# Optimization experiments

Measured on AMD Instinct MI355X. Metric: run time of the kernel, lower is better.

## Reference

```python
import jax, jax.numpy as jnp
import numpy as np

N, E, R, D, L, B, K = 50000, 800000, 64, 64, 4, 2, 32


def setup_inputs() -> dict:
    ks = jax.random.split(jax.random.key(0), 10)
    return {
        "edge_index": jax.random.randint(ks[0], (2, E), 0, N),
        "edge_type": jax.random.randint(ks[1], (E,), 0, R),
        "h_index": jax.random.randint(ks[2], (B,), 0, N),
        "r_index": jax.random.randint(ks[3], (B,), 0, R),
        "t_index": jax.random.randint(ks[4], (B, K), 0, N),
        "rel_repr": jax.random.normal(ks[5], (B, R, D)) * 0.1,
        "boundary_extra": jax.random.normal(ks[6], (B, N, D)) * 0.02,
        "layers_W": jax.random.normal(ks[7], (L, 2 * D, D)) / np.sqrt(2 * D),
        "layers_b": jnp.zeros((L, D)),
        "ln_g": jnp.ones((L, D)),
        "ln_b": jnp.zeros((L, D)),
        "w1": jax.random.normal(ks[8], (2 * D, D)) / np.sqrt(2 * D),
        "b1": jnp.zeros((D,)),
        "w2": jax.random.normal(ks[9], (D,)) / np.sqrt(D),
        "b2": jnp.zeros((1,)),
    }


def _layer_norm(x, g, b, eps=1e-5):
    mu = x.mean(-1, keepdims=True)
    var = ((x - mu) ** 2).mean(-1, keepdims=True)
    return (x - mu) * jax.lax.rsqrt(var + eps) * g + b


def reference(edge_index, edge_type, h_index, r_index, t_index, rel_repr,
              boundary_extra, layers_W, layers_b, ln_g, ln_b, w1, b1, w2, b2):
    src, dst = edge_index[0], edge_index[1]
    query = rel_repr[jnp.arange(B), r_index]  # [B, D] per-query relation embedding
    # enhanced boundary: entity/relation-enhanced base + query injected at head node
    boundary = boundary_extra.at[jnp.arange(B), h_index].add(query)  # [B, N, D]
    seg = jax.vmap(lambda m: jax.ops.segment_sum(m, dst, num_segments=N))
    x = boundary
    for l in range(L):
        msg = x[:, src, :] * rel_repr[:, edge_type, :]   # DistMult messages [B, E, D]
        agg = seg(msg) + boundary                        # sum aggregation + boundary self-message
        out = jnp.einsum('bnd,df->bnf', jnp.concatenate([x, agg], -1), layers_W[l]) + layers_b[l]
        out = jax.nn.relu(_layer_norm(out, ln_g[l], ln_b[l]))
        x = out + x                                      # short_cut residual
    node_feat = jnp.concatenate(
        [x, jnp.broadcast_to(query[:, None, :], (B, N, D))], axis=-1)  # [B, N, 2D]
    feat = node_feat[jnp.arange(B)[:, None], t_index]    # gather tails [B, K, 2D]
    h = jax.nn.relu(feat @ w1 + b1)
    score = h @ w2 + b2                                  # [B, K]
    return score
```

## Files before the change

### kernel.cpp

```cpp
#include <hip/hip_runtime.h>
#include <hip/hip_bf16.h>

#define NN 50000
#define EE 800000
#define RR 64
#define DD 64
#define LL 4
#define BB 2
#define KK 32

#define NBUK 98
#define BROWS 512
#define CHUNK 2048
#define NBLK 391
#define PLACE_CAP 10240
#define CAP3 8192

#define PB_REL   0
#define PB_WT    8192
#define PB_LB    40960
#define PB_G     41216
#define PB_BETA  41472
#define PB_W1    41728
#define PB_B1    49920
#define PB_W2    49984
#define PB_B2    50048
#define PB_TOT   50049

typedef short v8s __attribute__((ext_vector_type(8)));
typedef float v4f __attribute__((ext_vector_type(4)));
typedef _Float16 v2h __attribute__((ext_vector_type(2)));
typedef _Float16 v4h __attribute__((ext_vector_type(4)));
typedef unsigned short v4u __attribute__((ext_vector_type(4)));

static __device__ __forceinline__ float ldany(const void* p, int i, int flag) {
    if (flag) return __bfloat162float(((const __hip_bfloat16*)p)[i]);
    return ((const float*)p)[i];
}
static __device__ __forceinline__ unsigned short tobf(float x) {
    return (unsigned short)(__builtin_bit_cast(unsigned int, x) >> 16);
}
static __device__ __forceinline__ unsigned short rnebf(float x) {
    unsigned int u = __builtin_bit_cast(unsigned int, x);
    return (unsigned short)((u + 0x7FFFu + ((u >> 16) & 1u)) >> 16);
}
static __device__ __forceinline__ float frombf(unsigned short h) {
    return __builtin_bit_cast(float, ((unsigned int)h) << 16);
}
static __device__ __forceinline__ int getflag(const unsigned int* lng) {
    return (*lng == 0x3F803F80u) ? 1 : 0;
}

__global__ void k_prep(const void* __restrict__ rel, const void* __restrict__ lb,
                       const void* __restrict__ g, const void* __restrict__ beta,
                       const void* __restrict__ w1, const void* __restrict__ b1,
                       const void* __restrict__ w2, const void* __restrict__ b2,
                       const void* __restrict__ W, const unsigned int* __restrict__ lng,
                       float* __restrict__ pb, unsigned short* __restrict__ wshi,
                       unsigned short* __restrict__ wslo, _Float16* __restrict__ relH,
                       int* __restrict__ bucketCount, int* __restrict__ flag2,
                       int* __restrict__ flag3, int* __restrict__ cnts) {
    int gid = blockIdx.x * 256 + threadIdx.x;
    int flag = getflag(lng);
    if (gid < NBUK) bucketCount[gid] = 0;
    if (gid < NN) { flag2[gid] = 0; flag3[gid] = 0; }
    if (gid < 8) cnts[gid] = 0;
    if (gid < 32768) {
        int l = gid >> 13, r = gid & 8191, f = r >> 7, d = r & 127;
        float w = ldany(W, l * 8192 + d * 64 + f, flag);
        unsigned short h = tobf(w);
        wshi[gid] = h;
        wslo[gid] = tobf(w - frombf(h));
        if (gid < 8192) {
            int ty = gid >> 7, rr = gid & 127, dd = rr >> 1, b = rr & 1;
            relH[gid] = (_Float16)ldany(rel, b * 4096 + ty * 64 + dd, flag);
        }
    }
    if (gid >= PB_TOT) return;
    if (gid < PB_WT) { pb[gid] = ldany(rel, gid, flag); return; }
    if (gid < PB_LB) return;
    if (gid < PB_G)    { pb[gid] = ldany(lb,   gid - PB_LB,   flag); return; }
    if (gid < PB_BETA) { pb[gid] = ldany(g,    gid - PB_G,    flag); return; }
    if (gid < PB_W1)   { pb[gid] = ldany(beta, gid - PB_BETA, flag); return; }
    if (gid < PB_B1)   { pb[gid] = ldany(w1,   gid - PB_W1,   flag); return; }
    if (gid < PB_W2)   { pb[gid] = ldany(b1,   gid - PB_B1,   flag); return; }
    if (gid < PB_B2)   { pb[gid] = ldany(w2,   gid - PB_W2,   flag); return; }
    pb[gid] = ldany(b2, 0, flag);
}

__global__ void __launch_bounds__(256) k_bhist(const int* __restrict__ ei,
                                               int* __restrict__ bucketCount) {
    __shared__ int h[NBUK];
    int t = threadIdx.x;
    if (t < NBUK) h[t] = 0;
    __syncthreads();
    int base = blockIdx.x * CHUNK;
    #pragma unroll
    for (int i = 0; i < 8; ++i) {
        int e = base + i * 256 + t;
        if (e < EE) atomicAdd(&h[ei[EE + e] >> 9], 1);
    }
    __syncthreads();
    if (t < NBUK && h[t]) atomicAdd(&bucketCount[t], h[t]);
}

__global__ void k_bscan(const int* __restrict__ bucketCount,
                        int* __restrict__ bucketBase, int* __restrict__ bucketCursor) {
    __shared__ int s[128];
    int t = threadIdx.x;
    int v = (t < NBUK) ? bucketCount[t] : 0;
    s[t] = v;
    __syncthreads();
    for (int off = 1; off < 128; off <<= 1) {
        int a = (t >= off) ? s[t - off] : 0;
        __syncthreads();
        if (t >= off) s[t] += a;
        __syncthreads();
    }
    if (t < NBUK) {
        int b = s[t] - v;
        bucketBase[t] = b;
        bucketCursor[t] = b;
    }
    if (t == NBUK - 1) bucketBase[NBUK] = s[t];
}

__global__ void __launch_bounds__(256) k_bfill(const int* __restrict__ ei,
                                               const int* __restrict__ et,
                                               int* __restrict__ bucketCursor,
                                               unsigned int* __restrict__ btmp) {
    __shared__ int h[NBUK], rb[NBUK];
    int t = threadIdx.x;
    if (t < NBUK) h[t] = 0;
    __syncthreads();
    int base = blockIdx.x * CHUNK;
    unsigned int rec[8]; int bk[8];
    #pragma unroll
    for (int i = 0; i < 8; ++i) {
        int e = base + i * 256 + t;
        bk[i] = -1;
        if (e < EE) {
            int dst = ei[EE + e];
            rec[i] = (unsigned int)ei[e] | ((unsigned int)et[e] << 16)
                   | ((unsigned int)(dst & 511) << 22);
            bk[i] = dst >> 9;
            atomicAdd(&h[bk[i]], 1);
        }
    }
    __syncthreads();
    if (t < NBUK) rb[t] = h[t] ? atomicAdd(&bucketCursor[t], h[t]) : 0;
    __syncthreads();
    if (t < NBUK) h[t] = 0;
    __syncthreads();
    #pragma unroll
    for (int i = 0; i < 8; ++i) {
        if (bk[i] >= 0) {
            int pos = rb[bk[i]] + atomicAdd(&h[bk[i]], 1);
            btmp[pos] = rec[i];
        }
    }
}

__global__ void __launch_bounds__(256) k_place(const int* __restrict__ bucketBase,
                                               const unsigned int* __restrict__ btmp,
                                               unsigned int* __restrict__ elist,
                                               int* __restrict__ rowptr) {
    __shared__ int rp[BROWS + 1];
    __shared__ int cur[BROWS];
    __shared__ unsigned int outb[PLACE_CAP];
    int b = blockIdx.x, t = threadIdx.x;
    int base = bucketBase[b];
    int cnt  = bucketBase[b + 1] - base;

    for (int r = t; r < BROWS; r += 256) cur[r] = 0;
    __syncthreads();
    for (int i = t; i < cnt; i += 256) {
        unsigned int rec = btmp[base + i];
        atomicAdd(&cur[rec >> 22], 1);
    }
    __syncthreads();
    if (t < 64) {
        int lane = t;
        int loc[8]; int s = 0;
        #pragma unroll
        for (int j = 0; j < 8; ++j) { loc[j] = s; s += cur[lane * 8 + j]; }
        int inc = s;
        for (int off = 1; off < 64; off <<= 1) {
            int v = __shfl_up(inc, off, 64);
            if (lane >= off) inc += v;
        }
        int excl = inc - s;
        #pragma unroll
        for (int j = 0; j < 8; ++j) rp[lane * 8 + j] = excl + loc[j];
        if (lane == 63) rp[BROWS] = inc;
    }
    __syncthreads();
    for (int r = t; r < BROWS; r += 256) cur[r] = rp[r];
    __syncthreads();
    for (int i = t; i < cnt; i += 256) {
        unsigned int rec = btmp[base + i];
        int ld = rec >> 22;
        int pos = atomicAdd(&cur[ld], 1);
        outb[pos] = rec & 0x3FFFFFu;
    }
    __syncthreads();
    for (int i = t; i < cnt; i += 256) elist[base + i] = outb[i];
    for (int r = t; r < BROWS; r += 256) {
        int n = b * BROWS + r;
        if (n <= NN) rowptr[n] = base + rp[r];
    }
}

__global__ void k_setT(const int* __restrict__ t_index, int* __restrict__ flag3,
                       int* __restrict__ listT, int* __restrict__ cntT,
                       int* __restrict__ list3, int* __restrict__ cnt3) {
    int i = threadIdx.x;
    int t = t_index[i];
    if (atomicExch(&flag3[t], 1) == 0) {
        listT[atomicAdd(cntT, 1)] = t;
        list3[atomicAdd(cnt3, 1)] = t;
    }
}

__global__ void __launch_bounds__(256) k_set3(const int* __restrict__ rowptr,
                                              const unsigned int* __restrict__ elist,
                                              const int* __restrict__ listT,
                                              const int* __restrict__ cntT,
                                              int* __restrict__ flag3,
                                              int* __restrict__ list3,
                                              int* __restrict__ cnt3) {
    int wave = threadIdx.x >> 6, lane = threadIdx.x & 63;
    int idx = blockIdx.x * 4 + wave;
    if (idx >= *cntT) return;
    int n = listT[idx];
    int s0 = rowptr[n], s1 = rowptr[n + 1];
    for (int i = s0 + lane; i < s1; i += 64) {
        int src = (int)(elist[i] & 0xFFFFu);
        if (atomicExch(&flag3[src], 1) == 0) {
            int p = atomicAdd(cnt3, 1);
            if (p < CAP3) list3[p] = src;
        }
    }
}

__global__ void __launch_bounds__(256) k_set2(const int* __restrict__ rowptr,
                                              const unsigned int* __restrict__ elist,
                                              const int* __restrict__ list3,
                                              const int* __restrict__ cnt3,
                                              int* __restrict__ flag2,
                                              int* __restrict__ list2,
                                              int* __restrict__ cnt2) {
    int wave = threadIdx.x >> 6, lane = threadIdx.x & 63;
    int nw = gridDim.x * 4;
    int c3 = *cnt3;
    for (int idx = blockIdx.x * 4 + wave; idx < c3; idx += nw) {
        int n = list3[idx];
        if (lane == 0) {
            if (atomicExch(&flag2[n], 1) == 0) list2[atomicAdd(cnt2, 1)] = n;
        }
        int s0 = rowptr[n], s1 = rowptr[n + 1];
        for (int i = s0 + lane; i < s1; i += 64) {
            int src = (int)(elist[i] & 0xFFFFu);
            if (atomicExch(&flag2[src], 1) == 0) {
                list2[atomicAdd(cnt2, 1)] = src;
            }
        }
    }
}

__global__ void k_init(const void* __restrict__ be, const float* __restrict__ relf,
                       const int* __restrict__ h_index, const int* __restrict__ r_index,
                       const unsigned int* __restrict__ lng, _Float16* __restrict__ xH) {
    int idx = blockIdx.x * 256 + threadIdx.x;
    int flag = getflag(lng);
    int bn = idx >> 6;
    int d  = idx & 63;
    int b  = (bn >= NN) ? 1 : 0;
    int n  = bn - b * NN;
    float v = ldany(be, idx, flag);
    if (n == h_index[b]) v += relf[(b * RR + r_index[b]) * DD + d];
    xH[n * 128 + d * 2 + b] = (_Float16)v;
}

__global__ void __launch_bounds__(256) k_gather(const int* __restrict__ rowptr,
                                                const unsigned int* __restrict__ elist,
                                                const _Float16* __restrict__ xHin,
                                                const _Float16* __restrict__ relH,
                                                const void* __restrict__ be,
                                                const float* __restrict__ relf,
                                                const int* __restrict__ h_index,
                                                const int* __restrict__ r_index,
                                                const unsigned int* __restrict__ lng,
                                                const int* __restrict__ list,
                                                const int* __restrict__ cntp,
                                                unsigned short* __restrict__ aggH) {
    int wave = threadIdx.x >> 6, lane = threadIdx.x & 63;
    int idx = blockIdx.x * 4 + wave;
    int cnt = cntp ? *cntp : NN;
    if (idx >= cnt) return;
    int n = list ? list[idx] : idx;
    n = __builtin_amdgcn_readfirstlane(n);
    int start = __builtin_amdgcn_readfirstlane(rowptr[n]);
    int end   = __builtin_amdgcn_readfirstlane(rowptr[n + 1]);
    int flag  = getflag(lng);

    float a0 = ldany(be, n * DD + lane, flag);
    float a1 = ldany(be, (NN + n) * DD + lane, flag);
    if (n == h_index[0]) a0 += relf[(0 * RR + r_index[0]) * DD + lane];
    if (n == h_index[1]) a1 += relf[(1 * RR + r_index[1]) * DD + lane];

    for (int i = start; i < end; i += 8) {
        v2h xv[8], rv[8]; float mk[8];
        #pragma unroll
        for (int j = 0; j < 8; ++j) {
            int e = i + j;
            int ok = (e < end);
            unsigned int u = elist[ok ? e : start];
            int s = u & 0xFFFFu, ty = u >> 16;
            xv[j] = *(const v2h*)(xHin + s * 128 + lane * 2);
            rv[j] = *(const v2h*)(relH + ty * 128 + lane * 2);
            mk[j] = ok ? 1.f : 0.f;
        }
        #pragma unroll
        for (int j = 0; j < 8; ++j) {
            a0 += (float)xv[j].x * (float)rv[j].x * mk[j];
            a1 += (float)xv[j].y * (float)rv[j].y * mk[j];
        }
    }
    aggH[n * 64 + lane] = rnebf(a0);
    aggH[(NN + n) * 64 + lane] = rnebf(a1);
}

__global__ void __launch_bounds__(256) k_combine(const _Float16* __restrict__ xHin,
                                                 const unsigned short* __restrict__ aggH,
                                                 const unsigned short* __restrict__ whi,
                                                 const unsigned short* __restrict__ wlo,
                                                 const float* __restrict__ lb,
                                                 const float* __restrict__ g,
                                                 const float* __restrict__ beta,
                                                 const int* __restrict__ list,
                                                 const int* __restrict__ cntp,
                                                 _Float16* __restrict__ xHout) {
    __shared__ __attribute__((aligned(16))) unsigned short Xhi[64 * 136];
    __shared__ __attribute__((aligned(16))) unsigned short Xlo[64 * 72];
    __shared__ int nodes[32];
    float* outT = (float*)Xhi;

    int t = threadIdx.x;
    int cnt = cntp ? *cntp : NN;
    int ebase = blockIdx.x * 32;
    if (ebase >= cnt) return;

    if (t < 32) {
        int e = ebase + t;
        int ce = e < cnt ? e : cnt - 1;
        nodes[t] = list ? list[ce] : ce;
    }
    __syncthreads();

    #pragma unroll
    for (int it = 0; it < 4; ++it) {
        int idx = it * 256 + t;
        int nl = idx >> 5, j = idx & 31;
        int n = nodes[nl];
        v4h v = *(const v4h*)(xHin + (size_t)n * 128 + 4 * j);
        int r0 = nl, r1 = 32 + nl;
        int k0 = 2 * j, k1 = 2 * j + 1;
        float f; unsigned short h;
        f = (float)v.x; h = tobf(f); Xhi[r0 * 136 + k0] = h; Xlo[r0 * 72 + k0] = tobf(f - frombf(h));
        f = (float)v.y; h = tobf(f); Xhi[r1 * 136 + k0] = h; Xlo[r1 * 72 + k0] = tobf(f - frombf(h));
        f = (float)v.z; h = tobf(f); Xhi[r0 * 136 + k1] = h; Xlo[r0 * 72 + k1] = tobf(f - frombf(h));
        f = (float)v.w; h = tobf(f); Xhi[r1 * 136 + k1] = h; Xlo[r1 * 72 + k1] = tobf(f - frombf(h));
    }
    #pragma unroll
    for (int it = 0; it < 4; ++it) {
        int idx = it * 256 + t;
        int half = idx >> 9, rem = idx & 511;
        int nl = rem >> 4, j = rem & 15;
        int n = nodes[nl];
        v4u v = *(const v4u*)(aggH + (size_t)(half * NN + n) * 64 + 4 * j);
        int row = half * 32 + nl;
        int kb = 64 + 4 * j;
        Xhi[row * 136 + kb + 0] = v.x;
        Xhi[row * 136 + kb + 1] = v.y;
        Xhi[row * 136 + kb + 2] = v.z;
        Xhi[row * 136 + kb + 3] = v.w;
    }
    __syncthreads();

    int wave = t >> 6, lane = t & 63;
    int low = lane & 15, q = lane >> 4;

    v4f acc[4];
    #pragma unroll
    for (int ft = 0; ft < 4; ++ft) acc[ft] = 0.f;

    int arow = wave * 16 + low;
    #pragma unroll
    for (int kt = 0; kt < 2; ++kt) {
        int k0 = kt * 32 + q * 8;
        v8s ah = *(const v8s*)(Xhi + arow * 136 + k0);
        v8s al = *(const v8s*)(Xlo + arow * 72 + k0);
        #pragma unroll
        for (int ft = 0; ft < 4; ++ft) {
            v8s bh = *(const v8s*)(whi + (ft * 16 + low) * 128 + k0);
            v8s bl = *(const v8s*)(wlo + (ft * 16 + low) * 128 + k0);
            acc[ft] = __builtin_amdgcn_mfma_f32_16x16x32_bf16(ah, bh, acc[ft], 0, 0, 0);
            acc[ft] = __builtin_amdgcn_mfma_f32_16x16x32_bf16(al, bh, acc[ft], 0, 0, 0);
            acc[ft] = __builtin_amdgcn_mfma_f32_16x16x32_bf16(ah, bl, acc[ft], 0, 0, 0);
        }
    }
    #pragma unroll
    for (int kt = 2; kt < 4; ++kt) {
        int k0 = kt * 32 + q * 8;
        v8s ah = *(const v8s*)(Xhi + arow * 136 + k0);
        #pragma unroll
        for (int ft = 0; ft < 4; ++ft) {
            v8s bh = *(const v8s*)(whi + (ft * 16 + low) * 128 + k0);
            v8s bl = *(const v8s*)(wlo + (ft * 16 + low) * 128 + k0);
            acc[ft] = __builtin_amdgcn_mfma_f32_16x16x32_bf16(ah, bh, acc[ft], 0, 0, 0);
            acc[ft] = __builtin_amdgcn_mfma_f32_16x16x32_bf16(ah, bl, acc[ft], 0, 0, 0);
        }
    }

    float o[4][4];
    #pragma unroll
    for (int ft = 0; ft < 4; ++ft) {
        float lbv = lb[ft * 16 + low];
        #pragma unroll
        for (int r = 0; r < 4; ++r) o[ft][r] = acc[ft][r] + lbv;
    }
    float s1[4], s2[4];
    #pragma unroll
    for (int r = 0; r < 4; ++r) {
        s1[r] = o[0][r] + o[1][r] + o[2][r] + o[3][r];
        s2[r] = o[0][r]*o[0][r] + o[1][r]*o[1][r] + o[2][r]*o[2][r] + o[3][r]*o[3][r];
    }
    #pragma unroll
    for (int m = 1; m < 16; m <<= 1) {
        #pragma unroll
        for (int r = 0; r < 4; ++r) {
            s1[r] += __shfl_xor(s1[r], m, 64);
            s2[r] += __shfl_xor(s2[r], m, 64);
        }
    }
    float res[4][4];
    #pragma unroll
    for (int r = 0; r < 4; ++r) {
        int row = wave * 16 + q * 4 + r;
        float mu  = s1[r] * (1.f / 64.f);
        float var = s2[r] * (1.f / 64.f) - mu * mu;
        float rs  = rsqrtf(fmaxf(var, 0.f) + 1e-5f);
        #pragma unroll
        for (int ft = 0; ft < 4; ++ft) {
            int f = ft * 16 + low;
            float xold = frombf(Xhi[row * 136 + f]) + frombf(Xlo[row * 72 + f]);
            res[ft][r] = fmaxf((o[ft][r] - mu) * rs * g[f] + beta[f], 0.f) + xold;
        }
    }
    __syncthreads();

    #pragma unroll
    for (int r = 0; r < 4; ++r) {
        int row = wave * 16 + q * 4 + r;
        #pragma unroll
        for (int ft = 0; ft < 4; ++ft) outT[row * 65 + ft * 16 + low] = res[ft][r];
    }
    __syncthreads();

    #pragma unroll
    for (int it = 0; it < 4; ++it) {
        int idx = it * 256 + t;
        int nl = idx >> 5, j = idx & 31;
        if (ebase + nl < cnt) {
            int n = nodes[nl];
            v4h hv;
            hv.x = (_Float16)outT[nl * 65 + 2 * j];
            hv.y = (_Float16)outT[(32 + nl) * 65 + 2 * j];
            hv.z = (_Float16)outT[nl * 65 + 2 * j + 1];
            hv.w = (_Float16)outT[(32 + nl) * 65 + 2 * j + 1];
            *(v4h*)(xHout + (size_t)n * 128 + 4 * j) = hv;
        }
    }
}

__global__ void k_final(const _Float16* __restrict__ xH,
                        const float* __restrict__ relf,
                        const int* __restrict__ r_index,
                        const int* __restrict__ t_index,
                        const float* __restrict__ w1,
                        const float* __restrict__ b1,
                        const float* __restrict__ w2,
                        const float* __restrict__ b2,
                        const unsigned int* __restrict__ lng,
                        void* __restrict__ out) {
    int b = blockIdx.x >> 5;
    int k = blockIdx.x & 31;
    int f = threadIdx.x;
    int t = t_index[b * KK + k];
    const _Float16* xr = xH + (size_t)t * 128 + b;
    const float* q  = relf + (b * RR + r_index[b]) * DD;
    float acc = b1[f];
    #pragma unroll 8
    for (int d = 0; d < 64; ++d) acc += (float)xr[2 * d] * w1[d * 64 + f];
    #pragma unroll 8
    for (int d = 0; d < 64; ++d) acc += q[d] * w1[(64 + d) * 64 + f];
    float h = fmaxf(acc, 0.f);
    float p = h * w2[f];
    for (int m = 32; m > 0; m >>= 1) p += __shfl_xor(p, m, 64);
    if (f == 0) {
        float s = p + b2[0];
        if (getflag(lng)) ((__hip_bfloat16*)out)[b * KK + k] = __float2bfloat16(s);
        else              ((float*)out)[b * KK + k] = s;
    }
}

extern "C" void kernel_launch(void* const* d_in, const int* in_sizes, int n_in,
                              void* d_out, int out_size, void* d_ws, size_t ws_size,
                              hipStream_t stream) {
    const int* edge_index = (const int*)d_in[0];
    const int* edge_type  = (const int*)d_in[1];
    const int* h_index    = (const int*)d_in[2];
    const int* r_index    = (const int*)d_in[3];
    const int* t_index    = (const int*)d_in[4];
    const void* rel   = d_in[5];
    const void* be    = d_in[6];
    const void* lw    = d_in[7];
    const void* lbias = d_in[8];
    const void* lng   = d_in[9];
    const void* lnb   = d_in[10];
    const void* w1    = d_in[11];
    const void* b1    = d_in[12];
    const void* w2    = d_in[13];
    const void* b2    = d_in[14];

    _Float16* xHa = (_Float16*)d_ws;
    _Float16* xHb = xHa + (size_t)NN * 128;
    unsigned short* aggH = (unsigned short*)(xHb + (size_t)NN * 128);
    float*    pb  = (float*)(aggH + (size_t)BB * NN * 64);
    int*      ip  = (int*)(pb + PB_TOT);
    int*   rowptr       = ip;
    int*   bucketCount  = rowptr + NN + 1;
    int*   bucketBase   = bucketCount + NBUK;
    int*   bucketCursor = bucketBase + NBUK + 1;
    unsigned int* elist = (unsigned int*)(bucketCursor + NBUK);
    unsigned short* wshi = (unsigned short*)(elist + EE);
    unsigned short* wslo = wshi + 32768;
    _Float16* relH = (_Float16*)(wslo + 32768);
    int* flag2 = (int*)(relH + 8192);
    int* flag3 = flag2 + NN;
    int* listT = flag3 + NN;
    int* list3 = listT + 64;
    int* list2 = list3 + CAP3;
    int* cnts  = list2 + NN;
    unsigned int* btmp = (unsigned int*)xHb;
    const unsigned int* lngp = (const unsigned int*)lng;

    k_prep<<<196, 256, 0, stream>>>(rel, lbias, lng, lnb, w1, b1, w2, b2, lw,
                                    lngp, pb, wshi, wslo, relH, bucketCount,
                                    flag2, flag3, cnts);
    k_bhist<<<NBLK, 256, 0, stream>>>(edge_index, bucketCount);
    k_bscan<<<1, 128, 0, stream>>>(bucketCount, bucketBase, bucketCursor);
    k_bfill<<<NBLK, 256, 0, stream>>>(edge_index, edge_type, bucketCursor, btmp);
    k_place<<<NBUK, 256, 0, stream>>>(bucketBase, btmp, elist, rowptr);
    k_setT<<<1, 64, 0, stream>>>(t_index, flag3, listT, cnts + 0, list3, cnts + 1);
    k_set3<<<16, 256, 0, stream>>>(rowptr, elist, listT, cnts + 0, flag3, list3, cnts + 1);
    k_set2<<<256, 256, 0, stream>>>(rowptr, elist, list3, cnts + 1, flag2, list2, cnts + 2);
    k_init<<<25000, 256, 0, stream>>>(be, pb + PB_REL, h_index, r_index, lngp, xHa);

    const float* relf = pb + PB_REL;
    k_gather<<<12500, 256, 0, stream>>>(rowptr, elist, xHa, relH, be, relf,
                                        h_index, r_index, lngp, nullptr, nullptr, aggH);
    k_combine<<<1563, 256, 0, stream>>>(xHa, aggH, wshi + 0, wslo + 0,
                                        pb + PB_LB + 0, pb + PB_G + 0, pb + PB_BETA + 0,
                                        nullptr, nullptr, xHb);
    k_gather<<<12500, 256, 0, stream>>>(rowptr, elist, xHb, relH, be, relf,
                                        h_index, r_index, lngp, list2, cnts + 2, aggH);
    k_combine<<<1563, 256, 0, stream>>>(xHb, aggH, wshi + 8192, wslo + 8192,
                                        pb + PB_LB + 64, pb + PB_G + 64, pb + PB_BETA + 64,
                                        list2, cnts + 2, xHa);
    k_gather<<<2048, 256, 0, stream>>>(rowptr, elist, xHa, relH, be, relf,
                                       h_index, r_index, lngp, list3, cnts + 1, aggH);
    k_combine<<<256, 256, 0, stream>>>(xHa, aggH, wshi + 16384, wslo + 16384,
                                       pb + PB_LB + 128, pb + PB_G + 128, pb + PB_BETA + 128,
                                       list3, cnts + 1, xHb);
    k_gather<<<16, 256, 0, stream>>>(rowptr, elist, xHb, relH, be, relf,
                                     h_index, r_index, lngp, listT, cnts + 0, aggH);
    k_combine<<<2, 256, 0, stream>>>(xHb, aggH, wshi + 24576, wslo + 24576,
                                     pb + PB_LB + 192, pb + PB_G + 192, pb + PB_BETA + 192,
                                     listT, cnts + 0, xHa);
    k_final<<<64, 64, 0, stream>>>(xHa, pb + PB_REL, r_index, t_index,
                                   pb + PB_W1, pb + PB_B1, pb + PB_W2, pb + PB_B2,
                                   lngp, d_out);
}
```

Before: 340.9 us.

## Replace bucketed CSR build with degree-count scan and atomic scatter; fuse init into prep

Replaces the two-level bucket sort (histogram, bucket scan, bucket fill, per-bucket placement) with a per-node degree count, a three-pass prefix scan, and a direct atomic-cursor scatter into the edge list. The degree count and the vectorized boundary/x initialization are folded into the prep kernel as extra blocks. The two target-set kernels are merged into one, and flags are cleared with a memset. This cuts kernel launches and passes over the edges, but global atomics on per-node cursors give a nondeterministic edge order within each row and may contend more.

```diff
diff --git a/kernel.cpp b/kernel.cpp
--- a/kernel.cpp
+++ b/kernel.cpp
@@ -9,12 +9,13 @@
 #define BB 2
 #define KK 32
 
-#define NBUK 98
-#define BROWS 512
 #define CHUNK 2048
 #define NBLK 391
-#define PLACE_CAP 10240
 #define CAP3 8192
+
+#define PREP_BLKS 196
+#define INIT_BLKS 3125
+#define DEG_BLKS  391
 
 #define PB_REL   0
 #define PB_WT    8192
@@ -31,6 +32,7 @@
 typedef float v4f __attribute__((ext_vector_type(4)));
 typedef _Float16 v2h __attribute__((ext_vector_type(2)));
 typedef _Float16 v4h __attribute__((ext_vector_type(4)));
+typedef _Float16 v8h __attribute__((ext_vector_type(8)));
 typedef unsigned short v4u __attribute__((ext_vector_type(4)));
 
 static __device__ __forceinline__ float ldany(const void* p, int i, int flag) {
@@ -51,20 +53,65 @@
     return (*lng == 0x3F803F80u) ? 1 : 0;
 }
 
-__global__ void k_prep(const void* __restrict__ rel, const void* __restrict__ lb,
+__global__ void __launch_bounds__(256) k_prep(const void* __restrict__ rel, const void* __restrict__ lb,
                        const void* __restrict__ g, const void* __restrict__ beta,
                        const void* __restrict__ w1, const void* __restrict__ b1,
                        const void* __restrict__ w2, const void* __restrict__ b2,
                        const void* __restrict__ W, const unsigned int* __restrict__ lng,
+                       const void* __restrict__ be,
+                       const int* __restrict__ h_index, const int* __restrict__ r_index,
+                       const int* __restrict__ ei,
                        float* __restrict__ pb, unsigned short* __restrict__ wshi,
                        unsigned short* __restrict__ wslo, _Float16* __restrict__ relH,
-                       int* __restrict__ bucketCount, int* __restrict__ flag2,
-                       int* __restrict__ flag3, int* __restrict__ cnts) {
-    int gid = blockIdx.x * 256 + threadIdx.x;
+                       _Float16* __restrict__ xH, int* __restrict__ deg) {
+    int blk = blockIdx.x, t = threadIdx.x;
     int flag = getflag(lng);
-    if (gid < NBUK) bucketCount[gid] = 0;
-    if (gid < NN) { flag2[gid] = 0; flag3[gid] = 0; }
-    if (gid < 8) cnts[gid] = 0;
+
+    if (blk >= PREP_BLKS + INIT_BLKS) {
+        int base = (blk - PREP_BLKS - INIT_BLKS) * CHUNK;
+        #pragma unroll
+        for (int i = 0; i < 8; ++i) {
+            int e = base + i * 256 + t;
+            if (e < EE) atomicAdd(&deg[ei[EE + e]], 1);
+        }
+        return;
+    }
+    if (blk >= PREP_BLKS) {
+        int gid = (blk - PREP_BLKS) * 256 + t;
+        int n = gid >> 4, j = gid & 15, d0 = j * 4;
+        float x0[4], x1[4];
+        if (flag) {
+            v4u a = *(const v4u*)((const unsigned short*)be + (size_t)n * 64 + d0);
+            v4u bq = *(const v4u*)((const unsigned short*)be + (size_t)(NN + n) * 64 + d0);
+            #pragma unroll
+            for (int jj = 0; jj < 4; ++jj) { x0[jj] = frombf(a[jj]); x1[jj] = frombf(bq[jj]); }
+        } else {
+            v4f a = *(const v4f*)((const float*)be + (size_t)n * 64 + d0);
+            v4f bq = *(const v4f*)((const float*)be + (size_t)(NN + n) * 64 + d0);
+            #pragma unroll
+            for (int jj = 0; jj < 4; ++jj) { x0[jj] = a[jj]; x1[jj] = bq[jj]; }
+        }
+        if (n == h_index[0]) {
+            int r = r_index[0];
+            #pragma unroll
+            for (int jj = 0; jj < 4; ++jj) x0[jj] += ldany(rel, r * DD + d0 + jj, flag);
+        }
+        if (n == h_index[1]) {
+            int r = r_index[1];
+            #pragma unroll
+            for (int jj = 0; jj < 4; ++jj) x1[jj] += ldany(rel, (RR + r) * DD + d0 + jj, flag);
+        }
+        v8h o;
+        #pragma unroll
+        for (int jj = 0; jj < 4; ++jj) {
+            o[2 * jj]     = (_Float16)x0[jj];
+            o[2 * jj + 1] = (_Float16)x1[jj];
+        }
+        *(v8h*)(xH + (size_t)n * 128 + d0 * 2) = o;
+        return;
+    }
+
+    int gid = blk * 256 + t;
     if (gid < 32768) {
         int l = gid >> 13, r = gid & 8191, f = r >> 7, d = r & 127;
         float w = ldany(W, l * 8192 + d * 64 + f, flag);
@@ -88,159 +135,108 @@
     pb[gid] = ldany(b2, 0, flag);
 }
 
-__global__ void __launch_bounds__(256) k_bhist(const int* __restrict__ ei,
-                                               int* __restrict__ bucketCount) {
-    __shared__ int h[NBUK];
-    int t = threadIdx.x;
-    if (t < NBUK) h[t] = 0;
-    __syncthreads();
-    int base = blockIdx.x * CHUNK;
-    #pragma unroll
-    for (int i = 0; i < 8; ++i) {
-        int e = base + i * 256 + t;
-        if (e < EE) atomicAdd(&h[ei[EE + e] >> 9], 1);
-    }
-    __syncthreads();
-    if (t < NBUK && h[t]) atomicAdd(&bucketCount[t], h[t]);
-}
-
-__global__ void k_bscan(const int* __restrict__ bucketCount,
-                        int* __restrict__ bucketBase, int* __restrict__ bucketCursor) {
-    __shared__ int s[128];
-    int t = threadIdx.x;
-    int v = (t < NBUK) ? bucketCount[t] : 0;
+__global__ void __launch_bounds__(256) k_scan1(const int* __restrict__ deg,
+                                               int* __restrict__ cursor,
+                                               int* __restrict__ bsum) {
+    __shared__ int s[256];
+    int b = blockIdx.x, t = threadIdx.x;
+    int n = b * 256 + t;
+    int v = (n < NN) ? deg[n] : 0;
     s[t] = v;
     __syncthreads();
-    for (int off = 1; off < 128; off <<= 1) {
+    for (int off = 1; off < 256; off <<= 1) {
         int a = (t >= off) ? s[t - off] : 0;
         __syncthreads();
         if (t >= off) s[t] += a;
         __syncthreads();
     }
-    if (t < NBUK) {
-        int b = s[t] - v;
-        bucketBase[t] = b;
-        bucketCursor[t] = b;
-    }
-    if (t == NBUK - 1) bucketBase[NBUK] = s[t];
-}
-
-__global__ void __launch_bounds__(256) k_bfill(const int* __restrict__ ei,
-                                               const int* __restrict__ et,
-                                               int* __restrict__ bucketCursor,
-                                               unsigned int* __restrict__ btmp) {
-    __shared__ int h[NBUK], rb[NBUK];
+    if (n < NN) cursor[n] = s[t] - v;
+    if (t == 255) bsum[b] = s[255];
+}
+
+__global__ void k_scan2(const int* __restrict__ bsum, int* __restrict__ boff,
+                        int* __restrict__ rowptr) {
+    __shared__ int s[256];
     int t = threadIdx.x;
-    if (t < NBUK) h[t] = 0;
-    __syncthreads();
+    int v = (t < PREP_BLKS) ? bsum[t] : 0;
+    s[t] = v;
+    __syncthreads();
+    for (int off = 1; off < 256; off <<= 1) {
+        int a = (t >= off) ? s[t - off] : 0;
+        __syncthreads();
+        if (t >= off) s[t] += a;
+        __syncthreads();
+    }
+    if (t < PREP_BLKS) boff[t] = s[t] - v;
+    if (t == 0) rowptr[NN] = EE;
+}
+
+__global__ void __launch_bounds__(256) k_scan3(int* __restrict__ cursor,
+                                               const int* __restrict__ boff,
+                                               int* __restrict__ rowptr) {
+    int b = blockIdx.x, t = threadIdx.x;
+    int n = b * 256 + t;
+    if (n < NN) {
+        int r = cursor[n] + boff[b];
+        rowptr[n] = r;
+        cursor[n] = r;
+    }
+}
+
+__global__ void __launch_bounds__(256) k_scatter(const int* __restrict__ ei,
+                                                 const int* __restrict__ et,
+                                                 int* __restrict__ cursor,
+                                                 unsigned int* __restrict__ elist) {
+    int t = threadIdx.x;
     int base = blockIdx.x * CHUNK;
-    unsigned int rec[8]; int bk[8];
     #pragma unroll
     for (int i = 0; i < 8; ++i) {
         int e = base + i * 256 + t;
-        bk[i] = -1;
         if (e < EE) {
             int dst = ei[EE + e];
-            rec[i] = (unsigned int)ei[e] | ((unsigned int)et[e] << 16)
-                   | ((unsigned int)(dst & 511) << 22);
-            bk[i] = dst >> 9;
-            atomicAdd(&h[bk[i]], 1);
-        }
-    }
-    __syncthreads();
-    if (t < NBUK) rb[t] = h[t] ? atomicAdd(&bucketCursor[t], h[t]) : 0;
-    __syncthreads();
-    if (t < NBUK) h[t] = 0;
-    __syncthreads();
-    #pragma unroll
-    for (int i = 0; i < 8; ++i) {
-        if (bk[i] >= 0) {
-            int pos = rb[bk[i]] + atomicAdd(&h[bk[i]], 1);
-            btmp[pos] = rec[i];
-        }
-    }
-}
-
-__global__ void __launch_bounds__(256) k_place(const int* __restrict__ bucketBase,
-                                               const unsigned int* __restrict__ btmp,
-                                               unsigned int* __restrict__ elist,
-                                               int* __restrict__ rowptr) {
-    __shared__ int rp[BROWS + 1];
-    __shared__ int cur[BROWS];
-    __shared__ unsigned int outb[PLACE_CAP];
-    int b = blockIdx.x, t = threadIdx.x;
-    int base = bucketBase[b];
-    int cnt  = bucketBase[b + 1] - base;
-
-    for (int r = t; r < BROWS; r += 256) cur[r] = 0;
-    __syncthreads();
-    for (int i = t; i < cnt; i += 256) {
-        unsigned int rec = btmp[base + i];
-        atomicAdd(&cur[rec >> 22], 1);
-    }
+            unsigned int rec = (unsigned int)ei[e] | ((unsigned int)et[e] << 16);
+            int pos = atomicAdd(&cursor[dst], 1);
+            elist[pos] = rec;
+        }
+    }
+}
+
+__global__ void k_sets(const int* __restrict__ t_index,
+                       const int* __restrict__ rowptr,
+                       const unsigned int* __restrict__ elist,
+                       int* __restrict__ flag3,
+                       int* __restrict__ listT, int* __restrict__ list3,
+                       int* __restrict__ cnts) {
+    __shared__ int sT, s3;
+    __shared__ int lT[64];
+    int t = threadIdx.x;
+    if (t == 0) { sT = 0; s3 = 0; }
     __syncthreads();
     if (t < 64) {
-        int lane = t;
-        int loc[8]; int s = 0;
-        #pragma unroll
-        for (int j = 0; j < 8; ++j) { loc[j] = s; s += cur[lane * 8 + j]; }
-        int inc = s;
-        for (int off = 1; off < 64; off <<= 1) {
-            int v = __shfl_up(inc, off, 64);
-            if (lane >= off) inc += v;
-        }
-        int excl = inc - s;
-        #pragma unroll
-        for (int j = 0; j < 8; ++j) rp[lane * 8 + j] = excl + loc[j];
-        if (lane == 63) rp[BROWS] = inc;
-    }
-    __syncthreads();
-    for (int r = t; r < BROWS; r += 256) cur[r] = rp[r];
-    __syncthreads();
-    for (int i = t; i < cnt; i += 256) {
-        unsigned int rec = btmp[base + i];
-        int ld = rec >> 22;
-        int pos = atomicAdd(&cur[ld], 1);
-        outb[pos] = rec & 0x3FFFFFu;
-    }
-    __syncthreads();
-    for (int i = t; i < cnt; i += 256) elist[base + i] = outb[i];
-    for (int r = t; r < BROWS; r += 256) {
-        int n = b * BROWS + r;
-        if (n <= NN) rowptr[n] = base + rp[r];
-    }
-}
-
-__global__ void k_setT(const int* __restrict__ t_index, int* __restrict__ flag3,
-                       int* __restrict__ listT, int* __restrict__ cntT,
-                       int* __restrict__ list3, int* __restrict__ cnt3) {
-    int i = threadIdx.x;
-    int t = t_index[i];
-    if (atomicExch(&flag3[t], 1) == 0) {
-        listT[atomicAdd(cntT, 1)] = t;
-        list3[atomicAdd(cnt3, 1)] = t;
-    }
-}
-
-__global__ void __launch_bounds__(256) k_set3(const int* __restrict__ rowptr,
-                                              const unsigned int* __restrict__ elist,
-                                              const int* __restrict__ listT,
-                                              const int* __restrict__ cntT,
-                                              int* __restrict__ flag3,
-                                              int* __restrict__ list3,
-                                              int* __restrict__ cnt3) {
-    int wave = threadIdx.x >> 6, lane = threadIdx.x & 63;
-    int idx = blockIdx.x * 4 + wave;
-    if (idx >= *cntT) return;
-    int n = listT[idx];
-    int s0 = rowptr[n], s1 = rowptr[n + 1];
-    for (int i = s0 + lane; i < s1; i += 64) {
-        int src = (int)(elist[i] & 0xFFFFu);
-        if (atomicExch(&flag3[src], 1) == 0) {
-            int p = atomicAdd(cnt3, 1);
-            if (p < CAP3) list3[p] = src;
-        }
-    }
+        int n = t_index[t];
+        if (atomicExch(&flag3[n], 1) == 0) {
+            int p = atomicAdd(&sT, 1);
+            lT[p] = n; listT[p] = n; list3[p] = n;
+        }
+    }
+    __syncthreads();
+    int nT = sT;
+    if (t == 0) s3 = nT;
+    __syncthreads();
+    int wave = t >> 6, lane = t & 63;
+    for (int idx = wave; idx < nT; idx += 4) {
+        int n = lT[idx];
+        int s0 = rowptr[n], s1 = rowptr[n + 1];
+        for (int i = s0 + lane; i < s1; i += 64) {
+            int src = (int)(elist[i] & 0xFFFFu);
+            if (atomicExch(&flag3[src], 1) == 0) {
+                int p = atomicAdd(&s3, 1);
+                if (p < CAP3) list3[p] = src;
+            }
+        }
+    }
+    __syncthreads();
+    if (t == 0) { cnts[0] = nT; cnts[1] = (s3 > CAP3) ? CAP3 : s3; }
 }
 
 __global__ void __launch_bounds__(256) k_set2(const int* __restrict__ rowptr,
@@ -266,20 +262,6 @@
             }
         }
     }
-}
-
-__global__ void k_init(const void* __restrict__ be, const float* __restrict__ relf,
-                       const int* __restrict__ h_index, const int* __restrict__ r_index,
-                       const unsigned int* __restrict__ lng, _Float16* __restrict__ xH) {
-    int idx = blockIdx.x * 256 + threadIdx.x;
-    int flag = getflag(lng);
-    int bn = idx >> 6;
-    int d  = idx & 63;
-    int b  = (bn >= NN) ? 1 : 0;
-    int n  = bn - b * NN;
-    float v = ldany(be, idx, flag);
-    if (n == h_index[b]) v += relf[(b * RR + r_index[b]) * DD + d];
-    xH[n * 128 + d * 2 + b] = (_Float16)v;
 }
 
 __global__ void __launch_bounds__(256) k_gather(const int* __restrict__ rowptr,
@@ -539,34 +521,33 @@
     unsigned short* aggH = (unsigned short*)(xHb + (size_t)NN * 128);
     float*    pb  = (float*)(aggH + (size_t)BB * NN * 64);
     int*      ip  = (int*)(pb + PB_TOT);
-    int*   rowptr       = ip;
-    int*   bucketCount  = rowptr + NN + 1;
-    int*   bucketBase   = bucketCount + NBUK;
-    int*   bucketCursor = bucketBase + NBUK + 1;
-    unsigned int* elist = (unsigned int*)(bucketCursor + NBUK);
+    int* deg    = ip;
+    int* flag2  = deg + NN;
+    int* flag3  = flag2 + NN;
+    int* cnts   = flag3 + NN;
+    int* rowptr = cnts + 16;
+    int* cursor = rowptr + NN + 1;
+    int* bsum   = cursor + NN;
+    int* boff   = bsum + 256;
+    int* listT  = boff + 256;
+    int* list3  = listT + 64;
+    int* list2  = list3 + CAP3;
+    unsigned int* elist = (unsigned int*)(list2 + NN);
     unsigned short* wshi = (unsigned short*)(elist + EE);
     unsigned short* wslo = wshi + 32768;
     _Float16* relH = (_Float16*)(wslo + 32768);
-    int* flag2 = (int*)(relH + 8192);
-    int* flag3 = flag2 + NN;
-    int* listT = flag3 + NN;
-    int* list3 = listT + 64;
-    int* list2 = list3 + CAP3;
-    int* cnts  = list2 + NN;
-    unsigned int* btmp = (unsigned int*)xHb;
     const unsigned int* lngp = (const unsigned int*)lng;
 
-    k_prep<<<196, 256, 0, stream>>>(rel, lbias, lng, lnb, w1, b1, w2, b2, lw,
-                                    lngp, pb, wshi, wslo, relH, bucketCount,
-                                    flag2, flag3, cnts);
-    k_bhist<<<NBLK, 256, 0, stream>>>(edge_index, bucketCount);
-    k_bscan<<<1, 128, 0, stream>>>(bucketCount, bucketBase, bucketCursor);
-    k_bfill<<<NBLK, 256, 0, stream>>>(edge_index, edge_type, bucketCursor, btmp);
-    k_place<<<NBUK, 256, 0, stream>>>(bucketBase, btmp, elist, rowptr);
-    k_setT<<<1, 64, 0, stream>>>(t_index, flag3, listT, cnts + 0, list3, cnts + 1);
-    k_set3<<<16, 256, 0, stream>>>(rowptr, elist, listT, cnts + 0, flag3, list3, cnts + 1);
+    hipMemsetAsync(deg, 0, (size_t)(3 * NN + 16) * sizeof(int), stream);
+    k_prep<<<PREP_BLKS + INIT_BLKS + DEG_BLKS, 256, 0, stream>>>(
+        rel, lbias, lng, lnb, w1, b1, w2, b2, lw, lngp, be, h_index, r_index,
+        edge_index, pb, wshi, wslo, relH, xHa, deg);
+    k_scan1<<<PREP_BLKS, 256, 0, stream>>>(deg, cursor, bsum);
+    k_scan2<<<1, 256, 0, stream>>>(bsum, boff, rowptr);
+    k_scan3<<<PREP_BLKS, 256, 0, stream>>>(cursor, boff, rowptr);
+    k_scatter<<<NBLK, 256, 0, stream>>>(edge_index, edge_type, cursor, elist);
+    k_sets<<<1, 256, 0, stream>>>(t_index, rowptr, elist, flag3, listT, list3, cnts);
     k_set2<<<256, 256, 0, stream>>>(rowptr, elist, list3, cnts + 1, flag2, list2, cnts + 2);
-    k_init<<<25000, 256, 0, stream>>>(be, pb + PB_REL, h_index, r_index, lngp, xHa);
 
     const float* relf = pb + PB_REL;
     k_gather<<<12500, 256, 0, stream>>>(rowptr, elist, xHa, relH, be, relf,
```

Result: slower. 394.0 us (+15.6%).

## Merge prep, init and histogram kernels; fuse set kernels; use memset for zeroing

Applied to the files above, without the earlier changes.

Folds the boundary initialization (k_init) and the edge destination histogram (k_bhist) into k_prep as extra block ranges, and vectorizes the init so each thread writes 8 fp16 values instead of one. The k_setT and k_set3 kernels are merged into a single one-block kernel that uses shared-memory counters. Flag and counter zeroing moves to one hipMemsetAsync over a reordered workspace layout. The aim is to cut kernel launch count and per-launch gaps and to widen the init memory traffic. The trade-off is that set3 now runs on one block with four waves instead of sixteen blocks.

```diff
diff --git a/kernel.cpp b/kernel.cpp
--- a/kernel.cpp
+++ b/kernel.cpp
@@ -15,6 +15,10 @@
 #define NBLK 391
 #define PLACE_CAP 10240
 #define CAP3 8192
+
+#define PREP_BLKS 196
+#define INIT_BLKS 3125
+#define HIST_BLKS 391
 
 #define PB_REL   0
 #define PB_WT    8192
@@ -31,6 +35,7 @@
 typedef float v4f __attribute__((ext_vector_type(4)));
 typedef _Float16 v2h __attribute__((ext_vector_type(2)));
 typedef _Float16 v4h __attribute__((ext_vector_type(4)));
+typedef _Float16 v8h __attribute__((ext_vector_type(8)));
 typedef unsigned short v4u __attribute__((ext_vector_type(4)));
 
 static __device__ __forceinline__ float ldany(const void* p, int i, int flag) {
@@ -51,26 +56,76 @@
     return (*lng == 0x3F803F80u) ? 1 : 0;
 }
 
-__global__ void k_prep(const void* __restrict__ rel, const void* __restrict__ lb,
+__global__ void __launch_bounds__(256) k_prep(const void* __restrict__ rel, const void* __restrict__ lb,
                        const void* __restrict__ g, const void* __restrict__ beta,
                        const void* __restrict__ w1, const void* __restrict__ b1,
                        const void* __restrict__ w2, const void* __restrict__ b2,
                        const void* __restrict__ W, const unsigned int* __restrict__ lng,
+                       const void* __restrict__ be,
+                       const int* __restrict__ h_index, const int* __restrict__ r_index,
+                       const int* __restrict__ ei,
                        float* __restrict__ pb, unsigned short* __restrict__ wshi,
                        unsigned short* __restrict__ wslo, _Float16* __restrict__ relH,
-                       int* __restrict__ bucketCount, int* __restrict__ flag2,
-                       int* __restrict__ flag3, int* __restrict__ cnts) {
-    int gid = blockIdx.x * 256 + threadIdx.x;
+                       _Float16* __restrict__ xH, int* __restrict__ bucketCount) {
+    __shared__ int h[NBUK];
+    int blk = blockIdx.x, t = threadIdx.x;
     int flag = getflag(lng);
-    if (gid < NBUK) bucketCount[gid] = 0;
-    if (gid < NN) { flag2[gid] = 0; flag3[gid] = 0; }
-    if (gid < 8) cnts[gid] = 0;
+
+    if (blk >= PREP_BLKS + INIT_BLKS) {
+        if (t < NBUK) h[t] = 0;
+        __syncthreads();
+        int base = (blk - PREP_BLKS - INIT_BLKS) * CHUNK;
+        #pragma unroll
+        for (int i = 0; i < 8; ++i) {
+            int e = base + i * 256 + t;
+            if (e < EE) atomicAdd(&h[ei[EE + e] >> 9], 1);
+        }
+        __syncthreads();
+        if (t < NBUK && h[t]) atomicAdd(&bucketCount[t], h[t]);
+        return;
+    }
+    if (blk >= PREP_BLKS) {
+        int gid = (blk - PREP_BLKS) * 256 + t;
+        int n = gid >> 4, j = gid & 15, d0 = j * 4;
+        float x0[4], x1[4];
+        if (flag) {
+            v4u a = *(const v4u*)((const unsigned short*)be + (size_t)n * 64 + d0);
+            v4u bq = *(const v4u*)((const unsigned short*)be + (size_t)(NN + n) * 64 + d0);
+            #pragma unroll
+            for (int jj = 0; jj < 4; ++jj) { x0[jj] = frombf(a[jj]); x1[jj] = frombf(bq[jj]); }
+        } else {
+            v4f a = *(const v4f*)((const float*)be + (size_t)n * 64 + d0);
+            v4f bq = *(const v4f*)((const float*)be + (size_t)(NN + n) * 64 + d0);
+            #pragma unroll
+            for (int jj = 0; jj < 4; ++jj) { x0[jj] = a[jj]; x1[jj] = bq[jj]; }
+        }
+        if (n == h_index[0]) {
+            int r = r_index[0];
+            #pragma unroll
+            for (int jj = 0; jj < 4; ++jj) x0[jj] += ldany(rel, r * DD + d0 + jj, flag);
+        }
+        if (n == h_index[1]) {
+            int r = r_index[1];
+            #pragma unroll
+            for (int jj = 0; jj < 4; ++jj) x1[jj] += ldany(rel, (RR + r) * DD + d0 + jj, flag);
+        }
+        v8h o;
+        #pragma unroll
+        for (int jj = 0; jj < 4; ++jj) {
+            o[2 * jj]     = (_Float16)x0[jj];
+            o[2 * jj + 1] = (_Float16)x1[jj];
+        }
+        *(v8h*)(xH + (size_t)n * 128 + d0 * 2) = o;
+        return;
+    }
+
+    int gid = blk * 256 + t;
     if (gid < 32768) {
         int l = gid >> 13, r = gid & 8191, f = r >> 7, d = r & 127;
         float w = ldany(W, l * 8192 + d * 64 + f, flag);
-        unsigned short h = tobf(w);
-        wshi[gid] = h;
-        wslo[gid] = tobf(w - frombf(h));
+        unsigned short h2 = tobf(w);
+        wshi[gid] = h2;
+        wslo[gid] = tobf(w - frombf(h2));
         if (gid < 8192) {
             int ty = gid >> 7, rr = gid & 127, dd = rr >> 1, b = rr & 1;
             relH[gid] = (_Float16)ldany(rel, b * 4096 + ty * 64 + dd, flag);
@@ -88,22 +143,6 @@
     pb[gid] = ldany(b2, 0, flag);
 }
 
-__global__ void __launch_bounds__(256) k_bhist(const int* __restrict__ ei,
-                                               int* __restrict__ bucketCount) {
-    __shared__ int h[NBUK];
-    int t = threadIdx.x;
-    if (t < NBUK) h[t] = 0;
-    __syncthreads();
-    int base = blockIdx.x * CHUNK;
-    #pragma unroll
-    for (int i = 0; i < 8; ++i) {
-        int e = base + i * 256 + t;
-        if (e < EE) atomicAdd(&h[ei[EE + e] >> 9], 1);
-    }
-    __syncthreads();
-    if (t < NBUK && h[t]) atomicAdd(&bucketCount[t], h[t]);
-}
-
 __global__ void k_bscan(const int* __restrict__ bucketCount,
                         int* __restrict__ bucketBase, int* __restrict__ bucketCursor) {
     __shared__ int s[128];
@@ -211,36 +250,42 @@
     }
 }
 
-__global__ void k_setT(const int* __restrict__ t_index, int* __restrict__ flag3,
-                       int* __restrict__ listT, int* __restrict__ cntT,
-                       int* __restrict__ list3, int* __restrict__ cnt3) {
-    int i = threadIdx.x;
-    int t = t_index[i];
-    if (atomicExch(&flag3[t], 1) == 0) {
-        listT[atomicAdd(cntT, 1)] = t;
-        list3[atomicAdd(cnt3, 1)] = t;
-    }
-}
-
-__global__ void __launch_bounds__(256) k_set3(const int* __restrict__ rowptr,
-                                              const unsigned int* __restrict__ elist,
-                                              const int* __restrict__ listT,
-                                              const int* __restrict__ cntT,
-                                              int* __restrict__ flag3,
-                                              int* __restrict__ list3,
-                                              int* __restrict__ cnt3) {
-    int wave = threadIdx.x >> 6, lane = threadIdx.x & 63;
-    int idx = blockIdx.x * 4 + wave;
-    if (idx >= *cntT) return;
-    int n = listT[idx];
-    int s0 = rowptr[n], s1 = rowptr[n + 1];
-    for (int i = s0 + lane; i < s1; i += 64) {
-        int src = (int)(elist[i] & 0xFFFFu);
-        if (atomicExch(&flag3[src], 1) == 0) {
-            int p = atomicAdd(cnt3, 1);
-            if (p < CAP3) list3[p] = src;
-        }
-    }
+__global__ void k_sets(const int* __restrict__ t_index,
+                       const int* __restrict__ rowptr,
+                       const unsigned int* __restrict__ elist,
+                       int* __restrict__ flag3,
+                       int* __restrict__ listT, int* __restrict__ list3,
+                       int* __restrict__ cnts) {
+    __shared__ int sT, s3;
+    __shared__ int lT[64];
+    int t = threadIdx.x;
+    if (t == 0) { sT = 0; s3 = 0; }
+    __syncthreads();
+    if (t < 64) {
+        int n = t_index[t];
+        if (atomicExch(&flag3[n], 1) == 0) {
+            int p = atomicAdd(&sT, 1);
+            lT[p] = n; listT[p] = n; list3[p] = n;
+        }
+    }
+    __syncthreads();
+    int nT = sT;
+    if (t == 0) s3 = nT;
+    __syncthreads();
+    int wave = t >> 6, lane = t & 63;
+    for (int idx = wave; idx < nT; idx += 4) {
+        int n = lT[idx];
+        int s0 = rowptr[n], s1 = rowptr[n + 1];
+        for (int i = s0 + lane; i < s1; i += 64) {
+            int src = (int)(elist[i] & 0xFFFFu);
+            if (atomicExch(&flag3[src], 1) == 0) {
+                int p = atomicAdd(&s3, 1);
+                if (p < CAP3) list3[p] = src;
+            }
+        }
+    }
+    __syncthreads();
+    if (t == 0) { cnts[0] = nT; cnts[1] = (s3 > CAP3) ? CAP3 : s3; }
 }
 
 __global__ void __launch_bounds__(256) k_set2(const int* __restrict__ rowptr,
@@ -266,20 +311,6 @@
             }
         }
     }
-}
-
-__global__ void k_init(const void* __restrict__ be, const float* __restrict__ relf,
-                       const int* __restrict__ h_index, const int* __restrict__ r_index,
-                       const unsigned int* __restrict__ lng, _Float16* __restrict__ xH) {
-    int idx = blockIdx.x * 256 + threadIdx.x;
-    int flag = getflag(lng);
-    int bn = idx >> 6;
-    int d  = idx & 63;
-    int b  = (bn >= NN) ? 1 : 0;
-    int n  = bn - b * NN;
-    float v = ldany(be, idx, flag);
-    if (n == h_index[b]) v += relf[(b * RR + r_index[b]) * DD + d];
-    xH[n * 128 + d * 2 + b] = (_Float16)v;
 }
 
 __global__ void __launch_bounds__(256) k_gather(const int* __restrict__ rowptr,
@@ -539,34 +570,32 @@
     unsigned short* aggH = (unsigned short*)(xHb + (size_t)NN * 128);
     float*    pb  = (float*)(aggH + (size_t)BB * NN * 64);
     int*      ip  = (int*)(pb + PB_TOT);
-    int*   rowptr       = ip;
-    int*   bucketCount  = rowptr + NN + 1;
-    int*   bucketBase   = bucketCount + NBUK;
-    int*   bucketCursor = bucketBase + NBUK + 1;
-    unsigned int* elist = (unsigned int*)(bucketCursor + NBUK);
+    int* bucketCount = ip;
+    int* flag2  = bucketCount + NBUK;
+    int* flag3  = flag2 + NN;
+    int* cnts   = flag3 + NN;
+    int* rowptr = cnts + 16;
+    int* bucketBase   = rowptr + NN + 1;
+    int* bucketCursor = bucketBase + NBUK + 1;
+    int* listT  = bucketCursor + NBUK;
+    int* list3  = listT + 64;
+    int* list2  = list3 + CAP3;
+    unsigned int* elist = (unsigned int*)(list2 + NN);
     unsigned short* wshi = (unsigned short*)(elist + EE);
     unsigned short* wslo = wshi + 32768;
     _Float16* relH = (_Float16*)(wslo + 32768);
-    int* flag2 = (int*)(relH + 8192);
-    int* flag3 = flag2 + NN;
-    int* listT = flag3 + NN;
-    int* list3 = listT + 64;
-    int* list2 = list3 + CAP3;
-    int* cnts  = list2 + NN;
     unsigned int* btmp = (unsigned int*)xHb;
     const unsigned int* lngp = (const unsigned int*)lng;
 
-    k_prep<<<196, 256, 0, stream>>>(rel, lbias, lng, lnb, w1, b1, w2, b2, lw,
-                                    lngp, pb, wshi, wslo, relH, bucketCount,
-                                    flag2, flag3, cnts);
-    k_bhist<<<NBLK, 256, 0, stream>>>(edge_index, bucketCount);
+    hipMemsetAsync(bucketCount, 0, (size_t)(NBUK + 2 * NN + 16) * sizeof(int), stream);
+    k_prep<<<PREP_BLKS + INIT_BLKS + HIST_BLKS, 256, 0, stream>>>(
+        rel, lbias, lng, lnb, w1, b1, w2, b2, lw, lngp, be, h_index, r_index,
+        edge_index, pb, wshi, wslo, relH, xHa, bucketCount);
     k_bscan<<<1, 128, 0, stream>>>(bucketCount, bucketBase, bucketCursor);
     k_bfill<<<NBLK, 256, 0, stream>>>(edge_index, edge_type, bucketCursor, btmp);
     k_place<<<NBUK, 256, 0, stream>>>(bucketBase, btmp, elist, rowptr);
-    k_setT<<<1, 64, 0, stream>>>(t_index, flag3, listT, cnts + 0, list3, cnts + 1);
-    k_set3<<<16, 256, 0, stream>>>(rowptr, elist, listT, cnts + 0, flag3, list3, cnts + 1);
+    k_sets<<<1, 256, 0, stream>>>(t_index, rowptr, elist, flag3, listT, list3, cnts);
     k_set2<<<256, 256, 0, stream>>>(rowptr, elist, list3, cnts + 1, flag2, list2, cnts + 2);
-    k_init<<<25000, 256, 0, stream>>>(be, pb + PB_REL, h_index, r_index, lngp, xHa);
 
     const float* relf = pb + PB_REL;
     k_gather<<<12500, 256, 0, stream>>>(rowptr, elist, xHa, relH, be, relf,
```

Result: no change. 343.3 us (+0.7%).
